# Kernel optimization log

Hardware: AMD Instinct MI355X
Metric: run time of the kernel (lower is better)

## Reference

```python
import jax, jax.numpy as jnp
import numpy as np


def fwht(a, img_dim):
    # a: (B, C, N) with N = img_dim**2 a power of 2.
    # Sequential butterfly: log2(N) stages, each fully vectorized.
    B, C, N = a.shape
    h = 1
    while h < N:
        a = a.reshape(B, C, N // (2 * h), 2, h)
        x0 = a[..., 0, :]
        x1 = a[..., 1, :]
        a = jnp.stack([x0 + x1, x0 - x1], axis=-2)
        h *= 2
    return a.reshape(B, C, N) / img_dim


def setup_inputs() -> dict:
    key = jax.random.key(0)
    k1, k2 = jax.random.split(key)
    B, C, IMG, RATIO = 32, 3, 256, 4
    N = IMG * IMG  # 65536
    K = C * N // RATIO  # 49152
    vec = jax.random.normal(k1, (B, C * N), dtype=jnp.float32)
    singulars = jnp.ones((K,), dtype=jnp.float32)
    perm = jax.random.permutation(k2, N)  # int permutation of pixels
    return {"vec": vec, "singulars": singulars, "perm": perm,
            "channels": C, "img_dim": IMG}


def reference(vec, singulars, perm, channels, img_dim):
    # H(vec) = U(singulars * Vt(vec)[:, :K]) with U = identity reshape.
    B = vec.shape[0]
    N = img_dim * img_dim
    a = fwht(vec.reshape(B, channels, N), img_dim)         # (B, C, N)
    # Vt: gather permuted pixels, move channel last, flatten
    temp = a[:, :, perm].transpose(0, 2, 1).reshape(B, -1)  # (B, N*C)
    K = singulars.shape[0]
    return singulars * temp[:, :K]                          # (B, K)
```

## Files before the change

### kernel.cpp

```cpp
#include <hip/hip_runtime.h>

#define NTOT 65536
#define CCH 3
#define BB 32
#define KK 49152
#define JMAXV 16384
#define K1_FWHT 768
#define K1_TOTAL 1024

struct F3 { float x, y, z; };

__device__ __forceinline__ void bfly(float& a, float& b) {
    float s = a + b, d = a - b; a = s; b = d;
}

template<int CTRL>
__device__ __forceinline__ float dppx(float w) {
    return __uint_as_float((unsigned)__builtin_amdgcn_update_dpp(
        0, (int)__float_as_uint(w), CTRL, 0xF, 0xF, true));
}

struct Sg { float s1, s2, s4, s8, s16, s32; };

__device__ __forceinline__ float st1(float w, float s) {
    float p = dppx<0xB1>(w); return fmaf(s, w, p);
}
__device__ __forceinline__ float st2(float w, float s) {
    float p = dppx<0x4E>(w); return fmaf(s, w, p);
}
__device__ __forceinline__ float st4(float w, float s) {
    float p = dppx<0x141>(dppx<0x1B>(w)); return fmaf(s, w, p);
}
__device__ __forceinline__ float st8(float w, float s) {
    float p = dppx<0x140>(dppx<0x141>(w)); return fmaf(s, w, p);
}
__device__ __forceinline__ float st16(float w, float s) {
#if __has_builtin(__builtin_amdgcn_permlane16_swap)
    unsigned u = __float_as_uint(w);
    auto r = __builtin_amdgcn_permlane16_swap(u, u, false, false);
    return fmaf(s, __uint_as_float(r[1]), __uint_as_float(r[0]));
#else
    float p = __shfl_xor(w, 16); return fmaf(s, w, p);
#endif
}
__device__ __forceinline__ float st32(float w, float s) {
#if __has_builtin(__builtin_amdgcn_permlane32_swap)
    unsigned u = __float_as_uint(w);
    auto r = __builtin_amdgcn_permlane32_swap(u, u, false, false);
    return fmaf(s, __uint_as_float(r[1]), __uint_as_float(r[0]));
#else
    float p = __shfl_xor(w, 32); return fmaf(s, w, p);
#endif
}

__device__ __forceinline__ void lane_fwht6(float& w0, float& w1, float& w2,
                                           float& w3, const Sg& g) {
    w0 = st1(w0, g.s1);  w1 = st1(w1, g.s1);  w2 = st1(w2, g.s1);  w3 = st1(w3, g.s1);
    w0 = st2(w0, g.s2);  w1 = st2(w1, g.s2);  w2 = st2(w2, g.s2);  w3 = st2(w3, g.s2);
    w0 = st4(w0, g.s4);  w1 = st4(w1, g.s4);  w2 = st4(w2, g.s4);  w3 = st4(w3, g.s4);
    w0 = st8(w0, g.s8);  w1 = st8(w1, g.s8);  w2 = st8(w2, g.s8);  w3 = st8(w3, g.s8);
    w0 = st16(w0, g.s16); w1 = st16(w1, g.s16); w2 = st16(w2, g.s16); w3 = st16(w3, g.s16);
    w0 = st32(w0, g.s32); w1 = st32(w1, g.s32); w2 = st32(w2, g.s32); w3 = st32(w3, g.s32);
}

__device__ __forceinline__ Sg mk_signs(int lane) {
    Sg g;
    g.s1  = (lane & 1)  ? -1.0f : 1.0f;
    g.s2  = (lane & 2)  ? -1.0f : 1.0f;
    g.s4  = (lane & 4)  ? -1.0f : 1.0f;
    g.s8  = (lane & 8)  ? -1.0f : 1.0f;
    g.s16 = (lane & 16) ? -1.0f : 1.0f;
    g.s32 = (lane & 32) ? -1.0f : 1.0f;
    return g;
}

__device__ __forceinline__ unsigned short f2bf(float f) {
    return (unsigned short)((__float_as_uint(f) + 0x8000u) >> 16);
}

__global__ __launch_bounds__(256) void k1_lo_t(
        const float* __restrict__ vec, unsigned short* __restrict__ midt,
        const int* __restrict__ perm, int* __restrict__ jtabt) {
    __shared__ unsigned lds32[16 * 256];
    int bx = blockIdx.x, t = threadIdx.x;
    if (bx < K1_FWHT) {
        int rc  = bx >> 3;
        int hi0 = (bx & 7) * 32;
        const float* src = vec + (size_t)rc * NTOT;
        int lane = t & 63;
        int w    = t >> 6;
        Sg g = mk_signs(lane);
#pragma unroll
        for (int k = 0; k < 4; ++k) {
            int hi = hi0 + w * 8 + 2 * k;
            float4 a4 = *reinterpret_cast<const float4*>(src + (size_t)hi * 256 + 4 * lane);
            float4 b4 = *reinterpret_cast<const float4*>(src + (size_t)(hi + 1) * 256 + 4 * lane);
            float a0 = a4.x, a1 = a4.y, a2 = a4.z, a3 = a4.w;
            float b0 = b4.x, b1 = b4.y, b2 = b4.z, b3 = b4.w;

            bfly(a0, a1); bfly(a2, a3);
            bfly(a0, a2); bfly(a1, a3);
            lane_fwht6(a0, a1, a2, a3, g);
            bfly(b0, b1); bfly(b2, b3);
            bfly(b0, b2); bfly(b1, b3);
            lane_fwht6(b0, b1, b2, b3, g);

            int pi = w * 4 + k;
            uint4 pk;
            pk.x = (unsigned)f2bf(a0) | ((unsigned)f2bf(b0) << 16);
            pk.y = (unsigned)f2bf(a1) | ((unsigned)f2bf(b1) << 16);
            pk.z = (unsigned)f2bf(a2) | ((unsigned)f2bf(b2) << 16);
            pk.w = (unsigned)f2bf(a3) | ((unsigned)f2bf(b3) << 16);
            *reinterpret_cast<uint4*>(&lds32[pi * 256 + 4 * lane]) = pk;
        }
        __syncthreads();

        unsigned* d32 = reinterpret_cast<unsigned*>(
            midt + (size_t)rc * NTOT + (size_t)t * 256 + hi0);
#pragma unroll
        for (int q4 = 0; q4 < 4; ++q4) {
            uint4 v;
            v.x = lds32[(q4 * 4 + 0) * 256 + t];
            v.y = lds32[(q4 * 4 + 1) * 256 + t];
            v.z = lds32[(q4 * 4 + 2) * 256 + t];
            v.w = lds32[(q4 * 4 + 3) * 256 + t];
            reinterpret_cast<uint4*>(d32)[q4] = v;
        }
    } else {
        int j = (bx - K1_FWHT) * 256 + t;
        int n = perm[j];
        jtabt[(n & 255) * 256 + (n >> 8)] = (j < JMAXV) ? j : -1;
    }
}

__global__ __launch_bounds__(256) void k2_hi_scatter(
        const unsigned short* __restrict__ midt, const int* __restrict__ jtabt,
        const float* __restrict__ sing, float* __restrict__ out) {
    int gid  = blockIdx.x * 256 + threadIdx.x;
    int lane = gid & 63;
    int wid  = gid >> 6;
    int b    = wid >> 8;
    int lo   = wid & 255;
    Sg g = mk_signs(lane);

    float v[3][4];
#pragma unroll
    for (int c = 0; c < 3; ++c) {
        const uint2* p = reinterpret_cast<const uint2*>(
            midt + ((size_t)(b * 3 + c)) * NTOT + (size_t)lo * 256);
        uint2 u = p[lane];
        float w0 = __uint_as_float(u.x << 16);
        float w1 = __uint_as_float(u.x & 0xFFFF0000u);
        float w2 = __uint_as_float(u.y << 16);
        float w3 = __uint_as_float(u.y & 0xFFFF0000u);
        bfly(w0, w1); bfly(w2, w3);
        bfly(w0, w2); bfly(w1, w3);
        lane_fwht6(w0, w1, w2, w3, g);
        v[c][0] = w0; v[c][1] = w1; v[c][2] = w2; v[c][3] = w3;
    }

    int4 jq = reinterpret_cast<const int4*>(jtabt + (size_t)lo * 256)[lane];
    int jj[4] = { jq.x, jq.y, jq.z, jq.w };

    float* outb = out + (size_t)b * KK;
#pragma unroll
    for (int i = 0; i < 4; ++i) {
        int j = jj[i];
        if (j >= 0) {
            F3 s = *reinterpret_cast<const F3*>(sing + 3 * j);
            F3 o;
            o.x = (s.x * (1.0f / 256.0f)) * v[0][i];
            o.y = (s.y * (1.0f / 256.0f)) * v[1][i];
            o.z = (s.z * (1.0f / 256.0f)) * v[2][i];
            *reinterpret_cast<F3*>(outb + 3 * j) = o;
        }
    }
}

extern "C" void kernel_launch(void* const* d_in, const int* in_sizes, int n_in,
                              void* d_out, int out_size, void* d_ws, size_t ws_size,
                              hipStream_t stream) {
    const float* vec  = (const float*)d_in[0];
    const float* sing = (const float*)d_in[1];
    const int*   perm = (const int*)d_in[2];
    float* out = (float*)d_out;

    int*            jtabt = (int*)d_ws;
    unsigned short* midt  = (unsigned short*)((char*)d_ws + 262144);

    k1_lo_t<<<K1_TOTAL, 256, 0, stream>>>(vec, midt, perm, jtabt);
    k2_hi_scatter<<<BB * 256 / 4, 256, 0, stream>>>(midt, jtabt, sing, out);
}
```

Baseline: 25.34 us.

## Fuse both FWHT passes and gather into one LDS-resident kernel per image

Replaces the two-kernel pipeline (row FWHT to a transposed bf16 global buffer, then column FWHT and scatter) with one kernel that processes a whole 256x256 image per 1024-thread block in LDS. The bf16 image is held in padded shared memory, the second transform runs in place, and outputs are gathered via perm directly. This removes the global intermediate round trip, the jtab build and the second launch. In exchange it runs only 96 blocks with about 131KB LDS each, which leaves most of the GPU's CUs idle and serialises the load, transform and gather phases inside each block.

```diff
diff --git a/kernel.cpp b/kernel.cpp
--- a/kernel.cpp
+++ b/kernel.cpp
@@ -5,10 +5,10 @@
 #define BB 32
 #define KK 49152
 #define JMAXV 16384
-#define K1_FWHT 768
-#define K1_TOTAL 1024
-
-struct F3 { float x, y, z; };
+#define NBLK (BB * CCH)
+#define NTHR 1024
+#define PITCH 257
+#define LDS_BYTES (128 * PITCH * 4)
 
 __device__ __forceinline__ void bfly(float& a, float& b) {
     float s = a + b, d = a - b; a = s; b = d;
@@ -74,106 +74,72 @@
     return g;
 }
 
-__device__ __forceinline__ unsigned short f2bf(float f) {
-    return (unsigned short)((__float_as_uint(f) + 0x8000u) >> 16);
+__device__ __forceinline__ unsigned f2bf(float f) {
+    return (__float_as_uint(f) + 0x8000u) >> 16;
 }
+__device__ __forceinline__ float bfLo(unsigned u) { return __uint_as_float(u << 16); }
+__device__ __forceinline__ float bfHi(unsigned u) { return __uint_as_float(u & 0xFFFF0000u); }
 
-__global__ __launch_bounds__(256) void k1_lo_t(
-        const float* __restrict__ vec, unsigned short* __restrict__ midt,
-        const int* __restrict__ perm, int* __restrict__ jtabt) {
-    __shared__ unsigned lds32[16 * 256];
-    int bx = blockIdx.x, t = threadIdx.x;
-    if (bx < K1_FWHT) {
-        int rc  = bx >> 3;
-        int hi0 = (bx & 7) * 32;
-        const float* src = vec + (size_t)rc * NTOT;
-        int lane = t & 63;
-        int w    = t >> 6;
-        Sg g = mk_signs(lane);
-#pragma unroll
-        for (int k = 0; k < 4; ++k) {
-            int hi = hi0 + w * 8 + 2 * k;
-            float4 a4 = *reinterpret_cast<const float4*>(src + (size_t)hi * 256 + 4 * lane);
-            float4 b4 = *reinterpret_cast<const float4*>(src + (size_t)(hi + 1) * 256 + 4 * lane);
-            float a0 = a4.x, a1 = a4.y, a2 = a4.z, a3 = a4.w;
-            float b0 = b4.x, b1 = b4.y, b2 = b4.z, b3 = b4.w;
-
-            bfly(a0, a1); bfly(a2, a3);
-            bfly(a0, a2); bfly(a1, a3);
-            lane_fwht6(a0, a1, a2, a3, g);
-            bfly(b0, b1); bfly(b2, b3);
-            bfly(b0, b2); bfly(b1, b3);
-            lane_fwht6(b0, b1, b2, b3, g);
-
-            int pi = w * 4 + k;
-            uint4 pk;
-            pk.x = (unsigned)f2bf(a0) | ((unsigned)f2bf(b0) << 16);
-            pk.y = (unsigned)f2bf(a1) | ((unsigned)f2bf(b1) << 16);
-            pk.z = (unsigned)f2bf(a2) | ((unsigned)f2bf(b2) << 16);
-            pk.w = (unsigned)f2bf(a3) | ((unsigned)f2bf(b3) << 16);
-            *reinterpret_cast<uint4*>(&lds32[pi * 256 + 4 * lane]) = pk;
-        }
-        __syncthreads();
-
-        unsigned* d32 = reinterpret_cast<unsigned*>(
-            midt + (size_t)rc * NTOT + (size_t)t * 256 + hi0);
-#pragma unroll
-        for (int q4 = 0; q4 < 4; ++q4) {
-            uint4 v;
-            v.x = lds32[(q4 * 4 + 0) * 256 + t];
-            v.y = lds32[(q4 * 4 + 1) * 256 + t];
-            v.z = lds32[(q4 * 4 + 2) * 256 + t];
-            v.w = lds32[(q4 * 4 + 3) * 256 + t];
-            reinterpret_cast<uint4*>(d32)[q4] = v;
-        }
-    } else {
-        int j = (bx - K1_FWHT) * 256 + t;
-        int n = perm[j];
-        jtabt[(n & 255) * 256 + (n >> 8)] = (j < JMAXV) ? j : -1;
-    }
-}
-
-__global__ __launch_bounds__(256) void k2_hi_scatter(
-        const unsigned short* __restrict__ midt, const int* __restrict__ jtabt,
-        const float* __restrict__ sing, float* __restrict__ out) {
-    int gid  = blockIdx.x * 256 + threadIdx.x;
-    int lane = gid & 63;
-    int wid  = gid >> 6;
-    int b    = wid >> 8;
-    int lo   = wid & 255;
+__global__ __launch_bounds__(NTHR, 1) void whcs_fused(
+        const float* __restrict__ vec, const float* __restrict__ sing,
+        const int* __restrict__ perm, float* __restrict__ out) {
+    extern __shared__ unsigned lds[];
+    int rc   = blockIdx.x;
+    int t    = threadIdx.x;
+    int lane = t & 63;
+    int w    = t >> 6;
+    const float* src = vec + (size_t)rc * NTOT;
     Sg g = mk_signs(lane);
 
-    float v[3][4];
 #pragma unroll
-    for (int c = 0; c < 3; ++c) {
-        const uint2* p = reinterpret_cast<const uint2*>(
-            midt + ((size_t)(b * 3 + c)) * NTOT + (size_t)lo * 256);
-        uint2 u = p[lane];
-        float w0 = __uint_as_float(u.x << 16);
-        float w1 = __uint_as_float(u.x & 0xFFFF0000u);
-        float w2 = __uint_as_float(u.y << 16);
-        float w3 = __uint_as_float(u.y & 0xFFFF0000u);
+    for (int k = 0; k < 8; ++k) {
+        int pi = w * 8 + k;
+        const float* p0 = src + (size_t)(2 * pi) * 256 + 4 * lane;
+        float4 a4 = *reinterpret_cast<const float4*>(p0);
+        float4 b4 = *reinterpret_cast<const float4*>(p0 + 256);
+        float a0 = a4.x, a1 = a4.y, a2 = a4.z, a3 = a4.w;
+        float b0 = b4.x, b1 = b4.y, b2 = b4.z, b3 = b4.w;
+
+        bfly(a0, a1); bfly(a2, a3);
+        bfly(a0, a2); bfly(a1, a3);
+        lane_fwht6(a0, a1, a2, a3, g);
+        bfly(b0, b1); bfly(b2, b3);
+        bfly(b0, b2); bfly(b1, b3);
+        lane_fwht6(b0, b1, b2, b3, g);
+
+        uint4 pk;
+        pk.x = f2bf(a0) | (f2bf(b0) << 16);
+        pk.y = f2bf(a1) | (f2bf(b1) << 16);
+        pk.z = f2bf(a2) | (f2bf(b2) << 16);
+        pk.w = f2bf(a3) | (f2bf(b3) << 16);
+        *reinterpret_cast<uint4*>(&lds[pi * PITCH + 4 * lane]) = pk;
+    }
+    __syncthreads();
+
+#pragma unroll
+    for (int m = 0; m < 16; ++m) {
+        int lo = w * 16 + m;
+        unsigned u0 = lds[(2 * lane    ) * PITCH + lo];
+        unsigned u1 = lds[(2 * lane + 1) * PITCH + lo];
+        float w0 = bfLo(u0), w1 = bfHi(u0), w2 = bfLo(u1), w3 = bfHi(u1);
         bfly(w0, w1); bfly(w2, w3);
         bfly(w0, w2); bfly(w1, w3);
         lane_fwht6(w0, w1, w2, w3, g);
-        v[c][0] = w0; v[c][1] = w1; v[c][2] = w2; v[c][3] = w3;
+        lds[(2 * lane    ) * PITCH + lo] = f2bf(w0) | (f2bf(w1) << 16);
+        lds[(2 * lane + 1) * PITCH + lo] = f2bf(w2) | (f2bf(w3) << 16);
     }
+    __syncthreads();
 
-    int4 jq = reinterpret_cast<const int4*>(jtabt + (size_t)lo * 256)[lane];
-    int jj[4] = { jq.x, jq.y, jq.z, jq.w };
-
-    float* outb = out + (size_t)b * KK;
+    int b = rc / CCH, c = rc % CCH;
+    float* outp = out + (size_t)b * KK + c;
 #pragma unroll
-    for (int i = 0; i < 4; ++i) {
-        int j = jj[i];
-        if (j >= 0) {
-            F3 s = *reinterpret_cast<const F3*>(sing + 3 * j);
-            F3 o;
-            o.x = (s.x * (1.0f / 256.0f)) * v[0][i];
-            o.y = (s.y * (1.0f / 256.0f)) * v[1][i];
-            o.z = (s.z * (1.0f / 256.0f)) * v[2][i];
-            *reinterpret_cast<F3*>(outb + 3 * j) = o;
-        }
+    for (int it = 0; it < JMAXV / NTHR; ++it) {
+        int jj = it * NTHR + t;
+        int n  = perm[jj];
+        int lo = n & 255, hi = n >> 8;
+        unsigned u = lds[(hi >> 1) * PITCH + lo];
+        float val  = (hi & 1) ? bfHi(u) : bfLo(u);
+        outp[3 * jj] = sing[3 * jj + c] * (1.0f / 256.0f) * val;
     }
 }
 
@@ -185,9 +151,5 @@
     const int*   perm = (const int*)d_in[2];
     float* out = (float*)d_out;
 
-    int*            jtabt = (int*)d_ws;
-    unsigned short* midt  = (unsigned short*)((char*)d_ws + 262144);
-
-    k1_lo_t<<<K1_TOTAL, 256, 0, stream>>>(vec, midt, perm, jtabt);
-    k2_hi_scatter<<<BB * 256 / 4, 256, 0, stream>>>(midt, jtabt, sing, out);
+    whcs_fused<<<NBLK, NTHR, LDS_BYTES, stream>>>(vec, sing, perm, out);
 }
```

Result: slower. 32.90 us (+29.8%).
